# Optimization experiments

Hardware: AMD Instinct MI355X
Metric: run time of the kernel (lower is better)

Reference implementation:

```python
import jax, jax.numpy as jnp
import numpy as np

D_MODEL = 1024
N_HEADS = 16
HEAD_DIM = D_MODEL // N_HEADS


def setup_inputs() -> dict:
    key = jax.random.key(0)
    ks = jax.random.split(key, 5)
    B, L = 4, 2048
    x = jax.random.normal(ks[0], (B, L, D_MODEL), dtype=jnp.float32)
    s = 1.0 / np.sqrt(D_MODEL)
    W_qkv = jax.random.normal(ks[1], (D_MODEL, 3 * D_MODEL), dtype=jnp.float32) * s
    b_qkv = jnp.zeros((3 * D_MODEL,), dtype=jnp.float32)
    W_out = jax.random.normal(ks[2], (D_MODEL, D_MODEL), dtype=jnp.float32) * s
    b_out = jnp.zeros((D_MODEL,), dtype=jnp.float32)
    return {"x": x, "W_qkv": W_qkv, "b_qkv": b_qkv, "W_out": W_out, "b_out": b_out}


def reference(x, W_qkv, b_qkv, W_out, b_out):
    B, L, D = x.shape
    qkv = x @ W_qkv + b_qkv                      # [B, L, 3D]
    q, k, v = jnp.split(qkv, 3, axis=-1)
    def split_heads(t):
        return t.reshape(B, L, N_HEADS, HEAD_DIM).transpose(0, 2, 1, 3)  # [B,H,L,hd]
    q, k, v = split_heads(q), split_heads(k), split_heads(v)
    scale = 1.0 / np.sqrt(HEAD_DIM).astype(np.float32)
    scores = jnp.einsum('bhqd,bhkd->bhqk', q, k) * scale  # [B,H,L,L]
    causal = jnp.tril(jnp.ones((L, L), dtype=bool))       # True = keep
    scores = jnp.where(causal, scores, -jnp.inf)
    attn = jax.nn.softmax(scores, axis=-1)
    out = jnp.einsum('bhqk,bhkd->bhqd', attn, v)          # [B,H,L,hd]
    out = out.transpose(0, 2, 1, 3).reshape(B, L, D)
    return out @ W_out + b_out
```

## Files before the change

### kernel.cpp

```cpp
#include <hip/hip_runtime.h>
#include <hip/hip_bf16.h>
#include <stdint.h>

#define D_MODEL 1024
#define NH 16
#define HD 64
#define LSEQ 2048
#define BATCH 4
#define NROWS (BATCH * LSEQ)
#define SCALE_L2E 0.18033688011112042f

typedef __attribute__((ext_vector_type(8))) short s16x8;
typedef __attribute__((ext_vector_type(4))) float f32x4;
typedef __attribute__((ext_vector_type(4))) int   i32x4;

static __device__ __forceinline__ f32x4 mfma_bf16(s16x8 a, s16x8 b, f32x4 c) {
    return __builtin_amdgcn_mfma_f32_16x16x32_bf16(a, b, c, 0, 0, 0);
}

static __device__ __forceinline__ unsigned short f32_to_bf16(float f) {
    unsigned int u = __float_as_uint(f);
    u = (u + 0x7fffu + ((u >> 16) & 1u)) >> 16;
    return (unsigned short)u;
}

static __device__ __forceinline__ unsigned int cvtpk(float lo, float hi) {
    unsigned int r;
    asm("v_cvt_pk_bf16_f32 %0, %1, %2" : "=v"(r) : "v"(lo), "v"(hi));
    return r;
}

static __device__ __forceinline__ unsigned long long pack4(float a, float b,
                                                           float c, float d) {
    return (unsigned long long)cvtpk(a, b) |
           ((unsigned long long)cvtpk(c, d) << 32);
}

static __device__ __forceinline__ void gload16(const void* g, void* l) {
    __builtin_amdgcn_global_load_lds(
        (const __attribute__((address_space(1))) void*)g,
        (__attribute__((address_space(3))) void*)l, 16, 0, 0);
}


__global__ void cvt_f32_bf16(const float* __restrict__ in,
                             unsigned short* __restrict__ out, int n4) {
    int i = blockIdx.x * blockDim.x + threadIdx.x;
    if (i < n4) {
        float4 v = ((const float4*)in)[i];
        ushort4 o;
        o.x = f32_to_bf16(v.x); o.y = f32_to_bf16(v.y);
        o.z = f32_to_bf16(v.z); o.w = f32_to_bf16(v.w);
        ((ushort4*)out)[i] = o;
    }
}

__global__ __launch_bounds__(256) void transpose_cvt(
    const float* __restrict__ in, unsigned short* __restrict__ out, int K, int N) {
    __shared__ float tile[32][33];
    int n0 = blockIdx.x * 32, k0 = blockIdx.y * 32;
    int tx = threadIdx.x & 31, ty = threadIdx.x >> 5;
    #pragma unroll
    for (int i = 0; i < 4; i++) {
        int k = ty + i * 8;
        tile[k][tx] = in[(size_t)(k0 + k) * N + (n0 + tx)];
    }
    __syncthreads();
    #pragma unroll
    for (int i = 0; i < 4; i++) {
        int n = ty + i * 8;
        out[(size_t)(n0 + n) * K + (k0 + tx)] = f32_to_bf16(tile[tx][n]);
    }
}


__global__ __launch_bounds__(512, 2) void gemm256_qkv(
    const unsigned short* __restrict__ A,
    const unsigned short* __restrict__ Bt,
    const float* __restrict__ bias,
    unsigned short* __restrict__ q_buf, unsigned short* __restrict__ k_buf,
    unsigned short* __restrict__ vT) {
    extern __shared__ float4 smv[];
    char* sm = (char*)smv;
    const int K = 1024, NT = 16;
    const int tid = threadIdx.x;
    const int lane = tid & 63, w = tid >> 6;
    const int wm = w >> 2, wn = w & 3;
    const int lq = lane & 15, lk = lane >> 4;
    const int m0 = blockIdx.y * 256, n0 = blockIdx.x * 256;

    const unsigned short* GA = A + (size_t)m0 * K;
    const unsigned short* GB = Bt + (size_t)n0 * K;

    auto stage = [&](const unsigned short* G, int mat, int t, int half) {
        char* base = sm + (t & 1) * 65536 + mat * 32768 + half * 16384;
        const unsigned short* g0 = G + (size_t)(half * 128) * K + t * 64;
        #pragma unroll
        for (int j = 0; j < 2; j++) {
            int c = j * 512 + tid;
            int row = c >> 3, cc = c & 7;
            int cg = cc ^ (row & 7);
            gload16(g0 + (size_t)row * K + cg * 8,
                    base + (j * 512 + w * 64) * 16);
        }
    };
    auto lda = [&](int buf, int mf, int ks) -> s16x8 {
        int byte = (((mf * 16 + lq) * 128 + ks * 64 + lk * 16)) ^ ((lq & 7) << 4);
        return *(const s16x8*)(sm + buf * 65536 + wm * 16384 + byte);
    };
    auto ldb = [&](int buf, int nf, int ks) -> s16x8 {
        int byte = ((((wn & 1) * 64 + nf * 16 + lq) * 128 + ks * 64 + lk * 16)) ^
                   ((lq & 7) << 4);
        return *(const s16x8*)(sm + buf * 65536 + 32768 + (wn >> 1) * 16384 + byte);
    };

    f32x4 acc[8][4];
    #pragma unroll
    for (int m = 0; m < 8; m++)
        #pragma unroll
        for (int n = 0; n < 4; n++)
            #pragma unroll
            for (int r = 0; r < 4; r++) acc[m][n][r] = 0.f;

    stage(GA, 0, 0, 0); stage(GA, 0, 0, 1); stage(GB, 1, 0, 0); stage(GB, 1, 0, 1);
    stage(GA, 0, 1, 0); stage(GA, 0, 1, 1); stage(GB, 1, 1, 0);
    asm volatile("s_waitcnt vmcnt(6)" ::: "memory");
    __builtin_amdgcn_s_barrier();

    s16x8 alo[4][2], ahi[4][2], blo[2][2], bhi[2][2];
    for (int t = 0; t < NT; t++) {
        const int buf = t & 1;
        #pragma unroll
        for (int mf = 0; mf < 4; mf++)
            #pragma unroll
            for (int ks = 0; ks < 2; ks++) alo[mf][ks] = lda(buf, mf, ks);
        #pragma unroll
        for (int nf = 0; nf < 2; nf++)
            #pragma unroll
            for (int ks = 0; ks < 2; ks++) blo[nf][ks] = ldb(buf, nf, ks);
        if (t + 1 < NT) stage(GB, 1, t + 1, 1);
        __builtin_amdgcn_s_barrier();
        asm volatile("s_waitcnt lgkmcnt(0)" ::: "memory");
        __builtin_amdgcn_s_setprio(1);
        #pragma unroll
        for (int mf = 0; mf < 4; mf++)
            #pragma unroll
            for (int nf = 0; nf < 2; nf++)
                #pragma unroll
                for (int ks = 0; ks < 2; ks++)
                    acc[mf][nf] = mfma_bf16(alo[mf][ks], blo[nf][ks], acc[mf][nf]);
        __builtin_amdgcn_s_setprio(0);
        __builtin_amdgcn_s_barrier();
        #pragma unroll
        for (int nf = 0; nf < 2; nf++)
            #pragma unroll
            for (int ks = 0; ks < 2; ks++) bhi[nf][ks] = ldb(buf, 2 + nf, ks);
        __builtin_amdgcn_s_barrier();
        asm volatile("s_waitcnt lgkmcnt(0)" ::: "memory");
        __builtin_amdgcn_s_setprio(1);
        #pragma unroll
        for (int mf = 0; mf < 4; mf++)
            #pragma unroll
            for (int nf = 0; nf < 2; nf++)
                #pragma unroll
                for (int ks = 0; ks < 2; ks++)
                    acc[mf][2 + nf] = mfma_bf16(alo[mf][ks], bhi[nf][ks], acc[mf][2 + nf]);
        __builtin_amdgcn_s_setprio(0);
        __builtin_amdgcn_s_barrier();
        #pragma unroll
        for (int mf = 0; mf < 4; mf++)
            #pragma unroll
            for (int ks = 0; ks < 2; ks++) ahi[mf][ks] = lda(buf, 4 + mf, ks);
        if (t + 2 < NT) stage(GB, 1, t + 2, 0);
        __builtin_amdgcn_s_barrier();
        asm volatile("s_waitcnt lgkmcnt(0)" ::: "memory");
        __builtin_amdgcn_s_setprio(1);
        #pragma unroll
        for (int mf = 0; mf < 4; mf++)
            #pragma unroll
            for (int nf = 0; nf < 2; nf++)
                #pragma unroll
                for (int ks = 0; ks < 2; ks++)
                    acc[4 + mf][nf] = mfma_bf16(ahi[mf][ks], blo[nf][ks], acc[4 + mf][nf]);
        __builtin_amdgcn_s_setprio(0);
        __builtin_amdgcn_s_barrier();
        if (t + 2 < NT) { stage(GA, 0, t + 2, 0); stage(GA, 0, t + 2, 1); }
        __builtin_amdgcn_s_barrier();
        asm volatile("s_waitcnt lgkmcnt(0)" ::: "memory");
        __builtin_amdgcn_s_setprio(1);
        #pragma unroll
        for (int mf = 0; mf < 4; mf++)
            #pragma unroll
            for (int nf = 0; nf < 2; nf++)
                #pragma unroll
                for (int ks = 0; ks < 2; ks++)
                    acc[4 + mf][2 + nf] = mfma_bf16(ahi[mf][ks], bhi[nf][ks], acc[4 + mf][2 + nf]);
        __builtin_amdgcn_s_setprio(0);
        if (t + 2 < NT) {
            asm volatile("s_waitcnt vmcnt(6)" ::: "memory");
        } else if (t + 1 < NT) {
            asm volatile("s_waitcnt vmcnt(0)" ::: "memory");
        }
        __builtin_amdgcn_s_barrier();
    }

    const int rowb = m0 + wm * 128 + lk * 4;
    const int colb = n0 + wn * 64 + lq;
    if (n0 < 1024) {
        #pragma unroll
        for (int mf = 0; mf < 8; mf++) {
            int row = rowb + mf * 16;
            #pragma unroll
            for (int nf = 0; nf < 4; nf++) {
                int col = colb + nf * 16;
                float bv = bias[col];
                #pragma unroll
                for (int r = 0; r < 4; r++)
                    q_buf[(size_t)(row + r) * 1024 + col] =
                        f32_to_bf16((acc[mf][nf][r] + bv) * SCALE_L2E);
            }
        }
    } else if (n0 < 2048) {
        #pragma unroll
        for (int mf = 0; mf < 8; mf++) {
            int row = rowb + mf * 16;
            #pragma unroll
            for (int nf = 0; nf < 4; nf++) {
                int col = colb + nf * 16;
                float bv = bias[col];
                #pragma unroll
                for (int r = 0; r < 4; r++)
                    k_buf[(size_t)(row + r) * 1024 + (col - 1024)] =
                        f32_to_bf16(acc[mf][nf][r] + bv);
            }
        }
    } else {
        #pragma unroll
        for (int mf = 0; mf < 8; mf++) {
            int row = rowb + mf * 16;
            int bb = row >> 11, pos = row & 2047;
            #pragma unroll
            for (int nf = 0; nf < 4; nf++) {
                int col = colb + nf * 16;
                int dg = col - 2048;
                float bv = bias[col];
                unsigned long long pk =
                    pack4(acc[mf][nf][0] + bv, acc[mf][nf][1] + bv,
                          acc[mf][nf][2] + bv, acc[mf][nf][3] + bv);
                *(unsigned long long*)(vT +
                    ((size_t)((bb * 16 + (dg >> 6)) * 64 + (dg & 63))) * 2048 + pos) = pk;
            }
        }
    }
}


__global__ __launch_bounds__(256) void gemm_bf16_f32(
    const unsigned short* __restrict__ A,
    const unsigned short* __restrict__ Bt,
    const float* __restrict__ bias,
    float* __restrict__ C, int M, int N, int K) {
    __shared__ __align__(16) unsigned short As[2][128][32];
    __shared__ __align__(16) unsigned short Bs[2][128][32];

    const int tid = threadIdx.x;
    const int m0 = blockIdx.y * 128;
    const int n0 = blockIdx.x * 128;
    const int lane = tid & 63, w4 = tid >> 6;
    const int wr = w4 >> 1, wc = w4 & 1;
    const int lq = lane & 15, lk = lane >> 4;

    const int srow = lane >> 2;
    const int sk = (lane & 3) * 8;
    const unsigned short* ap = A  + (size_t)(m0 + w4 * 16 + srow) * K + sk;
    const unsigned short* bp = Bt + (size_t)(n0 + w4 * 16 + srow) * K + sk;

    f32x4 acc[4][4];
    #pragma unroll
    for (int m = 0; m < 4; m++)
        #pragma unroll
        for (int n = 0; n < 4; n++)
            #pragma unroll
            for (int r = 0; r < 4; r++) acc[m][n][r] = 0.f;

    gload16(ap,                  &As[0][w4 * 16][0]);
    gload16(ap + (size_t)64 * K, &As[0][64 + w4 * 16][0]);
    gload16(bp,                  &Bs[0][w4 * 16][0]);
    gload16(bp + (size_t)64 * K, &Bs[0][64 + w4 * 16][0]);
    __syncthreads();

    int buf = 0;
    for (int k0 = 0; k0 < K; k0 += 32) {
        if (k0 + 32 < K) {
            const unsigned short* ap2 = ap + k0 + 32;
            const unsigned short* bp2 = bp + k0 + 32;
            gload16(ap2,                  &As[buf ^ 1][w4 * 16][0]);
            gload16(ap2 + (size_t)64 * K, &As[buf ^ 1][64 + w4 * 16][0]);
            gload16(bp2,                  &Bs[buf ^ 1][w4 * 16][0]);
            gload16(bp2 + (size_t)64 * K, &Bs[buf ^ 1][64 + w4 * 16][0]);
        }
        s16x8 af[4], bfr[4];
        #pragma unroll
        for (int m = 0; m < 4; m++)
            af[m] = *(const s16x8*)(&As[buf][wr * 64 + m * 16 + lq][lk * 8]);
        #pragma unroll
        for (int n = 0; n < 4; n++)
            bfr[n] = *(const s16x8*)(&Bs[buf][wc * 64 + n * 16 + lq][lk * 8]);
        #pragma unroll
        for (int m = 0; m < 4; m++)
            #pragma unroll
            for (int n = 0; n < 4; n++)
                acc[m][n] = mfma_bf16(af[m], bfr[n], acc[m][n]);
        __syncthreads();
        buf ^= 1;
    }

    #pragma unroll
    for (int m = 0; m < 4; m++) {
        int row = m0 + wr * 64 + m * 16 + lk * 4;
        #pragma unroll
        for (int n = 0; n < 4; n++) {
            int col = n0 + wc * 64 + n * 16 + lq;
            float bv = bias[col];
            #pragma unroll
            for (int r = 0; r < 4; r++)
                C[(size_t)(row + r) * N + col] = acc[m][n][r] + bv;
        }
    }
}


__global__ __launch_bounds__(256) void attn_kernel(
    const unsigned short* __restrict__ q_buf,
    const unsigned short* __restrict__ k_buf,
    const unsigned short* __restrict__ vT,
    unsigned short* __restrict__ out) {
    __shared__ __align__(16) char lds[24576];
    char* Ks = lds;
    char* Vs = lds + 8192;

    const int bid = blockIdx.x;
    const int bh = bid & 63;
    const int pj = bid >> 6;
    const int b = bh >> 4, h = bh & 15;
    const int tid = threadIdx.x, lane = tid & 63, w = tid >> 6;
    const int lq = lane & 15, lk = lane >> 4;
    char* Pw = lds + 16384 + w * 2048;

    const int srow = tid >> 3, sch = tid & 7;
    const int sby0 = (srow * 128 + sch * 16) ^ ((srow & 7) << 4);
    const int sby1 = ((srow + 32) * 128 + sch * 16) ^ ((srow & 7) << 4);
    const int swzA = (lq & 7) << 4;

    const unsigned short* kbase =
        k_buf + (size_t)b * LSEQ * 1024 + h * 64 + (size_t)srow * 1024 + sch * 8;
    const unsigned short* vbase =
        vT + (size_t)bh * 64 * 2048 + (size_t)srow * 2048 + sch * 8;

    auto run_stream = [&](int qtile, int nkv) {
        const int q_g = qtile * 64 + w * 16 + lq;
        const unsigned short* qp = q_buf + ((size_t)b * LSEQ + q_g) * 1024 + h * 64;
        const s16x8 qf0 = *(const s16x8*)(qp + lk * 8);
        const s16x8 qf1 = *(const s16x8*)(qp + 32 + lk * 8);

        const unsigned short* kp = kbase;
        const unsigned short* vp = vbase;

        float m_r = -1e30f, l_r = 0.f;
        f32x4 o[4];
        #pragma unroll
        for (int n = 0; n < 4; n++)
            #pragma unroll
            for (int r = 0; r < 4; r++) o[n][r] = 0.f;

        i32x4 r0 = *(const i32x4*)kp;
        i32x4 r1 = *(const i32x4*)(kp + (size_t)32 * 1024);
        i32x4 r2 = *(const i32x4*)vp;
        i32x4 r3 = *(const i32x4*)(vp + (size_t)32 * 2048);

        for (int kvb = 0; kvb < nkv; kvb++) {
            *(i32x4*)(Ks + sby0) = r0;
            *(i32x4*)(Ks + sby1) = r1;
            *(i32x4*)(Vs + sby0) = r2;
            *(i32x4*)(Vs + sby1) = r3;
            __syncthreads();
            if (kvb + 1 < nkv) {
                kp += 64 * 1024;
                vp += 64;
                r0 = *(const i32x4*)kp;
                r1 = *(const i32x4*)(kp + (size_t)32 * 1024);
                r2 = *(const i32x4*)vp;
                r3 = *(const i32x4*)(vp + (size_t)32 * 2048);
            }

            f32x4 sT[4];
            #pragma unroll
            for (int n = 0; n < 4; n++)
                #pragma unroll
                for (int r = 0; r < 4; r++) sT[n][r] = 0.f;
            __builtin_amdgcn_s_setprio(1);
            #pragma unroll
            for (int n = 0; n < 4; n++) {
                const int rb = (n * 16 + lq) * 128;
                s16x8 a0 = *(const s16x8*)(Ks + ((rb + lk * 16) ^ swzA));
                s16x8 a1 = *(const s16x8*)(Ks + ((rb + 64 + lk * 16) ^ swzA));
                sT[n] = mfma_bf16(a0, qf0, sT[n]);
                sT[n] = mfma_bf16(a1, qf1, sT[n]);
            }
            __builtin_amdgcn_s_setprio(0);
            if (kvb == nkv - 1) {
                const int kv0 = kvb * 64;
                #pragma unroll
                for (int n = 0; n < 4; n++)
                    #pragma unroll
                    for (int r = 0; r < 4; r++)
                        if (kv0 + n * 16 + lk * 4 + r > q_g) sT[n][r] = -1e30f;
            }

            float mx = sT[0][0];
            #pragma unroll
            for (int n = 0; n < 4; n++)
                #pragma unroll
                for (int r = 0; r < 4; r++) mx = fmaxf(mx, sT[n][r]);
            mx = fmaxf(mx, __shfl_xor(mx, 16, 64));
            mx = fmaxf(mx, __shfl_xor(mx, 32, 64));
            if (!__all(mx <= m_r + 8.f)) {
                const float mnew = fmaxf(m_r, mx);
                const float corr = __builtin_amdgcn_exp2f(m_r - mnew);
                m_r = mnew;
                l_r *= corr;
                #pragma unroll
                for (int n = 0; n < 4; n++)
                    #pragma unroll
                    for (int r = 0; r < 4; r++) o[n][r] *= corr;
            }
            float sum = 0.f;
            unsigned long long pk[4];
            #pragma unroll
            for (int n = 0; n < 4; n++) {
                float p0 = __builtin_amdgcn_exp2f(sT[n][0] - m_r);
                float p1 = __builtin_amdgcn_exp2f(sT[n][1] - m_r);
                float p2 = __builtin_amdgcn_exp2f(sT[n][2] - m_r);
                float p3 = __builtin_amdgcn_exp2f(sT[n][3] - m_r);
                sum += (p0 + p1) + (p2 + p3);
                pk[n] = pack4(p0, p1, p2, p3);
            }
            l_r += sum;

            #pragma unroll
            for (int n = 0; n < 4; n++)
                *(unsigned long long*)(Pw + ((lq * 128 + n * 32 + lk * 8) ^ swzA)) = pk[n];
            asm volatile("s_waitcnt lgkmcnt(0)" ::: "memory");

            __builtin_amdgcn_s_setprio(1);
            #pragma unroll
            for (int kk = 0; kk < 2; kk++) {
                s16x8 pb = *(const s16x8*)(Pw + ((lq * 128 + kk * 64 + lk * 16) ^ swzA));
                #pragma unroll
                for (int n = 0; n < 4; n++) {
                    s16x8 vf = *(const s16x8*)(Vs +
                        (((n * 16 + lq) * 128 + kk * 64 + lk * 16) ^ swzA));
                    o[n] = mfma_bf16(vf, pb, o[n]);
                }
            }
            __builtin_amdgcn_s_setprio(0);
            asm volatile("s_barrier" ::: "memory");
        }

        l_r += __shfl_xor(l_r, 16, 64);
        l_r += __shfl_xor(l_r, 32, 64);
        const float inv = 1.f / l_r;
        unsigned short* op = out + ((size_t)b * LSEQ + q_g) * 1024 + h * 64;
        #pragma unroll
        for (int n = 0; n < 4; n++) {
            *(unsigned long long*)(op + n * 16 + lk * 4) =
                pack4(o[n][0] * inv, o[n][1] * inv, o[n][2] * inv, o[n][3] * inv);
        }
    };

    run_stream(31 - pj, 32 - pj);
    run_stream(pj, pj + 1);
}


extern "C" void kernel_launch(void* const* d_in, const int* in_sizes, int n_in,
                              void* d_out, int out_size, void* d_ws, size_t ws_size,
                              hipStream_t stream) {
    const float* x     = (const float*)d_in[0];
    const float* W_qkv = (const float*)d_in[1];
    const float* b_qkv = (const float*)d_in[2];
    const float* W_out = (const float*)d_in[3];
    const float* b_out = (const float*)d_in[4];
    float* out = (float*)d_out;

    char* p = (char*)d_ws;
    unsigned short* x_bf   = (unsigned short*)p; p += (size_t)NROWS * D_MODEL * 2;
    unsigned short* wqkv_t = (unsigned short*)p; p += (size_t)3 * D_MODEL * D_MODEL * 2;
    unsigned short* wout_t = (unsigned short*)p; p += (size_t)D_MODEL * D_MODEL * 2;
    unsigned short* q_buf  = (unsigned short*)p; p += (size_t)NROWS * D_MODEL * 2;
    unsigned short* k_buf  = (unsigned short*)p; p += (size_t)NROWS * D_MODEL * 2;
    unsigned short* vT     = (unsigned short*)p; p += (size_t)NROWS * D_MODEL * 2;
    unsigned short* attn   = (unsigned short*)p;

    hipFuncSetAttribute((const void*)gemm256_qkv,
                        hipFuncAttributeMaxDynamicSharedMemorySize, 131072);

    int n4 = NROWS * D_MODEL / 4;
    hipLaunchKernelGGL(cvt_f32_bf16, dim3((n4 + 255) / 256), dim3(256), 0, stream,
                       x, x_bf, n4);
    hipLaunchKernelGGL(transpose_cvt, dim3(3 * D_MODEL / 32, D_MODEL / 32), dim3(256),
                       0, stream, W_qkv, wqkv_t, D_MODEL, 3 * D_MODEL);
    hipLaunchKernelGGL(transpose_cvt, dim3(D_MODEL / 32, D_MODEL / 32), dim3(256),
                       0, stream, W_out, wout_t, D_MODEL, D_MODEL);
    hipLaunchKernelGGL(gemm256_qkv, dim3(3 * D_MODEL / 256, NROWS / 256),
                       dim3(512), 131072, stream, x_bf, wqkv_t, b_qkv,
                       q_buf, k_buf, vT);
    hipLaunchKernelGGL(attn_kernel, dim3(16 * 64), dim3(256), 0, stream,
                       q_buf, k_buf, vT, attn);
    hipLaunchKernelGGL(gemm_bf16_f32, dim3(D_MODEL / 128, NROWS / 128),
                       dim3(256), 0, stream, attn, wout_t, b_out, out,
                       NROWS, D_MODEL, D_MODEL);
}
```

Baseline: 272.6 us.

## Merge prep kernels, remap GEMM block order for XCD locality, tree-reduce max

Fuses the three preprocessing kernels (x conversion and two weight transpose-converts) into a single launch to remove launch gaps. Both GEMMs remap block indices so consecutive blocks are spread across the eight XCDs in a chunked order, aiming for better L2 reuse of shared A/B tiles. The attention row-max becomes a shallower tree reduction, and the bf16 packing switches to uint2 stores. The risk is that the grid-stride x conversion in prep uses fewer blocks per element, and that the swizzle only helps if the hardware dispatches blocks round-robin across XCDs.

```diff
diff --git a/kernel.cpp b/kernel.cpp
--- a/kernel.cpp
+++ b/kernel.cpp
@@ -30,10 +30,12 @@
     return r;
 }
 
-static __device__ __forceinline__ unsigned long long pack4(float a, float b,
-                                                           float c, float d) {
-    return (unsigned long long)cvtpk(a, b) |
-           ((unsigned long long)cvtpk(c, d) << 32);
+static __device__ __forceinline__ void store_bf16x4(void* p, float a, float b,
+                                                    float c, float d) {
+    uint2 t;
+    t.x = cvtpk(a, b);
+    t.y = cvtpk(c, d);
+    *(uint2*)p = t;
 }
 
 static __device__ __forceinline__ void gload16(const void* g, void* l) {
@@ -43,22 +45,9 @@
 }
 
 
-__global__ void cvt_f32_bf16(const float* __restrict__ in,
-                             unsigned short* __restrict__ out, int n4) {
-    int i = blockIdx.x * blockDim.x + threadIdx.x;
-    if (i < n4) {
-        float4 v = ((const float4*)in)[i];
-        ushort4 o;
-        o.x = f32_to_bf16(v.x); o.y = f32_to_bf16(v.y);
-        o.z = f32_to_bf16(v.z); o.w = f32_to_bf16(v.w);
-        ((ushort4*)out)[i] = o;
-    }
-}
-
-__global__ __launch_bounds__(256) void transpose_cvt(
-    const float* __restrict__ in, unsigned short* __restrict__ out, int K, int N) {
-    __shared__ float tile[32][33];
-    int n0 = blockIdx.x * 32, k0 = blockIdx.y * 32;
+static __device__ __forceinline__ void transpose_tile(
+    const float* __restrict__ in, unsigned short* __restrict__ out,
+    int K, int N, int n0, int k0, float (*tile)[33]) {
     int tx = threadIdx.x & 31, ty = threadIdx.x >> 5;
     #pragma unroll
     for (int i = 0; i < 4; i++) {
@@ -70,6 +59,33 @@
     for (int i = 0; i < 4; i++) {
         int n = ty + i * 8;
         out[(size_t)(n0 + n) * K + (k0 + tx)] = f32_to_bf16(tile[tx][n]);
+    }
+}
+
+__global__ __launch_bounds__(256) void prep_kernel(
+    const float* __restrict__ x, const float* __restrict__ W_qkv,
+    const float* __restrict__ W_out,
+    unsigned short* __restrict__ x_bf, unsigned short* __restrict__ wqkv_t,
+    unsigned short* __restrict__ wout_t) {
+    __shared__ float tile[32][33];
+    const int bid = blockIdx.x;
+    if (bid < 3072) {
+        transpose_tile(W_qkv, wqkv_t, 1024, 3072, (bid % 96) * 32,
+                       (bid / 96) * 32, tile);
+    } else if (bid < 4096) {
+        int t = bid - 3072;
+        transpose_tile(W_out, wout_t, 1024, 1024, (t % 32) * 32,
+                       (t / 32) * 32, tile);
+    } else {
+        const int t = bid - 4096;
+        const int n4 = NROWS * D_MODEL / 4;
+        for (int i = t * 256 + (int)threadIdx.x; i < n4; i += 2048 * 256) {
+            float4 v = ((const float4*)x)[i];
+            ushort4 o;
+            o.x = f32_to_bf16(v.x); o.y = f32_to_bf16(v.y);
+            o.z = f32_to_bf16(v.z); o.w = f32_to_bf16(v.w);
+            ((ushort4*)x_bf)[i] = o;
+        }
     }
 }
 
@@ -87,7 +103,9 @@
     const int lane = tid & 63, w = tid >> 6;
     const int wm = w >> 2, wn = w & 3;
     const int lq = lane & 15, lk = lane >> 4;
-    const int m0 = blockIdx.y * 256, n0 = blockIdx.x * 256;
+    int bid0 = blockIdx.y * 12 + blockIdx.x;
+    bid0 = (bid0 & 7) * 48 + (bid0 >> 3);
+    const int m0 = (bid0 / 12) * 256, n0 = (bid0 % 12) * 256;
 
     const unsigned short* GA = A + (size_t)m0 * K;
     const unsigned short* GB = Bt + (size_t)n0 * K;
@@ -244,11 +262,10 @@
                 int col = colb + nf * 16;
                 int dg = col - 2048;
                 float bv = bias[col];
-                unsigned long long pk =
-                    pack4(acc[mf][nf][0] + bv, acc[mf][nf][1] + bv,
-                          acc[mf][nf][2] + bv, acc[mf][nf][3] + bv);
-                *(unsigned long long*)(vT +
-                    ((size_t)((bb * 16 + (dg >> 6)) * 64 + (dg & 63))) * 2048 + pos) = pk;
+                store_bf16x4(vT +
+                    ((size_t)((bb * 16 + (dg >> 6)) * 64 + (dg & 63))) * 2048 + pos,
+                    acc[mf][nf][0] + bv, acc[mf][nf][1] + bv,
+                    acc[mf][nf][2] + bv, acc[mf][nf][3] + bv);
             }
         }
     }
@@ -264,8 +281,10 @@
     __shared__ __align__(16) unsigned short Bs[2][128][32];
 
     const int tid = threadIdx.x;
-    const int m0 = blockIdx.y * 128;
-    const int n0 = blockIdx.x * 128;
+    int bid0 = blockIdx.y * 8 + blockIdx.x;
+    bid0 = (bid0 & 7) * 64 + (bid0 >> 3);
+    const int m0 = (bid0 >> 3) * 128;
+    const int n0 = (bid0 & 7) * 128;
     const int lane = tid & 63, w4 = tid >> 6;
     const int wr = w4 >> 1, wc = w4 & 1;
     const int lq = lane & 15, lk = lane >> 4;
@@ -417,11 +436,13 @@
                         if (kv0 + n * 16 + lk * 4 + r > q_g) sT[n][r] = -1e30f;
             }
 
-            float mx = sT[0][0];
-            #pragma unroll
-            for (int n = 0; n < 4; n++)
-                #pragma unroll
-                for (int r = 0; r < 4; r++) mx = fmaxf(mx, sT[n][r]);
+            float a0 = fmaxf(fmaxf(sT[0][0], sT[0][1]), sT[0][2]);
+            float a1 = fmaxf(fmaxf(sT[0][3], sT[1][0]), sT[1][1]);
+            float a2 = fmaxf(fmaxf(sT[1][2], sT[1][3]), sT[2][0]);
+            float a3 = fmaxf(fmaxf(sT[2][1], sT[2][2]), sT[2][3]);
+            float a4 = fmaxf(fmaxf(sT[3][0], sT[3][1]), sT[3][2]);
+            float mx = fmaxf(fmaxf(fmaxf(a0, a1), a2),
+                             fmaxf(fmaxf(a3, a4), sT[3][3]));
             mx = fmaxf(mx, __shfl_xor(mx, 16, 64));
             mx = fmaxf(mx, __shfl_xor(mx, 32, 64));
             if (!__all(mx <= m_r + 8.f)) {
@@ -435,7 +456,7 @@
                     for (int r = 0; r < 4; r++) o[n][r] *= corr;
             }
             float sum = 0.f;
-            unsigned long long pk[4];
+            uint2 pk[4];
             #pragma unroll
             for (int n = 0; n < 4; n++) {
                 float p0 = __builtin_amdgcn_exp2f(sT[n][0] - m_r);
@@ -443,13 +464,14 @@
                 float p2 = __builtin_amdgcn_exp2f(sT[n][2] - m_r);
                 float p3 = __builtin_amdgcn_exp2f(sT[n][3] - m_r);
                 sum += (p0 + p1) + (p2 + p3);
-                pk[n] = pack4(p0, p1, p2, p3);
+                pk[n].x = cvtpk(p0, p1);
+                pk[n].y = cvtpk(p2, p3);
             }
             l_r += sum;
 
             #pragma unroll
             for (int n = 0; n < 4; n++)
-                *(unsigned long long*)(Pw + ((lq * 128 + n * 32 + lk * 8) ^ swzA)) = pk[n];
+                *(uint2*)(Pw + ((lq * 128 + n * 32 + lk * 8) ^ swzA)) = pk[n];
             asm volatile("s_waitcnt lgkmcnt(0)" ::: "memory");
 
             __builtin_amdgcn_s_setprio(1);
@@ -472,10 +494,9 @@
         const float inv = 1.f / l_r;
         unsigned short* op = out + ((size_t)b * LSEQ + q_g) * 1024 + h * 64;
         #pragma unroll
-        for (int n = 0; n < 4; n++) {
-            *(unsigned long long*)(op + n * 16 + lk * 4) =
-                pack4(o[n][0] * inv, o[n][1] * inv, o[n][2] * inv, o[n][3] * inv);
-        }
+        for (int n = 0; n < 4; n++)
+            store_bf16x4(op + n * 16 + lk * 4, o[n][0] * inv, o[n][1] * inv,
+                         o[n][2] * inv, o[n][3] * inv);
     };
 
     run_stream(31 - pj, 32 - pj);
@@ -505,13 +526,8 @@
     hipFuncSetAttribute((const void*)gemm256_qkv,
                         hipFuncAttributeMaxDynamicSharedMemorySize, 131072);
 
-    int n4 = NROWS * D_MODEL / 4;
-    hipLaunchKernelGGL(cvt_f32_bf16, dim3((n4 + 255) / 256), dim3(256), 0, stream,
-                       x, x_bf, n4);
-    hipLaunchKernelGGL(transpose_cvt, dim3(3 * D_MODEL / 32, D_MODEL / 32), dim3(256),
-                       0, stream, W_qkv, wqkv_t, D_MODEL, 3 * D_MODEL);
-    hipLaunchKernelGGL(transpose_cvt, dim3(D_MODEL / 32, D_MODEL / 32), dim3(256),
-                       0, stream, W_out, wout_t, D_MODEL, D_MODEL);
+    hipLaunchKernelGGL(prep_kernel, dim3(6144), dim3(256), 0, stream,
+                       x, W_qkv, W_out, x_bf, wqkv_t, wout_t);
     hipLaunchKernelGGL(gemm256_qkv, dim3(3 * D_MODEL / 256, NROWS / 256),
                        dim3(512), 131072, stream, x_bf, wqkv_t, b_qkv,
                        q_buf, k_buf, vT);
```

Result: faster. 264.9 us (-2.8%).
